# Optimization experiments

Hardware: AMD Instinct MI355X
Metric: run time of the kernel (lower is better)

## Reference

```python
import jax, jax.numpy as jnp
import numpy as np

NL, NH, H, FF, V, P = 12, 12, 768, 3072, 30522, 512
B, L, S = 4, 512, 8
DH = H // NH


def _layer_norm(x, g, b, eps=1e-12):
    m = x.mean(-1, keepdims=True)
    v = jnp.mean((x - m) ** 2, axis=-1, keepdims=True)
    return (x - m) * jax.lax.rsqrt(v + eps) * g + b


def setup_inputs() -> dict:
    key = jax.random.key(0)
    ks = iter(jax.random.split(key, 40))
    pm = lambda shape: jax.random.normal(next(ks), shape, jnp.float32) * 0.02
    inp = {
        'word_emb': pm((V, H)), 'pos_emb': pm((P, H)), 'type_emb': pm((2, H)),
        'emb_ln_g': jnp.ones((H,), jnp.float32), 'emb_ln_b': jnp.zeros((H,), jnp.float32),
        'Wq': pm((NL, H, H)), 'bq': jnp.zeros((NL, H), jnp.float32),
        'Wk': pm((NL, H, H)), 'bk': jnp.zeros((NL, H), jnp.float32),
        'Wv': pm((NL, H, H)), 'bv': jnp.zeros((NL, H), jnp.float32),
        'Wo': pm((NL, H, H)), 'bo': jnp.zeros((NL, H), jnp.float32),
        'attn_ln_g': jnp.ones((NL, H), jnp.float32), 'attn_ln_b': jnp.zeros((NL, H), jnp.float32),
        'W1': pm((NL, H, FF)), 'b1': jnp.zeros((NL, FF), jnp.float32),
        'W2': pm((NL, FF, H)), 'b2': jnp.zeros((NL, H), jnp.float32),
        'ffn_ln_g': jnp.ones((NL, H), jnp.float32), 'ffn_ln_b': jnp.zeros((NL, H), jnp.float32),
        'fc_w': pm((H,)), 'fc_b': jnp.zeros((), jnp.float32),
    }
    inp['input_ids'] = jax.random.randint(next(ks), (B, L), 0, V)
    inp['token_type_ids'] = jnp.zeros((B, L), jnp.int32)
    # valid-length prefix attention_mask and sorted bos_locations (history = 64)
    vl = np.array([384 + 16 * (i % 8) for i in range(B)])
    hist = 64
    am = (np.arange(L)[None, :] < vl[:, None]).astype(np.int32)
    bos = np.stack([hist + (np.arange(S) * (v - hist)) // S for v in vl]).astype(np.int64)
    inp['attention_mask'] = jnp.asarray(am)
    inp['bos_locations'] = jnp.asarray(bos)
    return inp


def _forward(word_emb, pos_emb, type_emb, emb_ln_g, emb_ln_b,
             Wq, bq, Wk, bk, Wv, bv, Wo, bo, attn_ln_g, attn_ln_b,
             W1, b1, W2, b2, ffn_ln_g, ffn_ln_b, fc_w, fc_b,
             input_ids, token_type_ids, attention_mask, bos_locations):
    Bs, Ls = input_ids.shape
    t = jnp.arange(Ls)
    valid_len = attention_mask.sum(-1)                       # [B]
    hist = bos_locations[:, 0]                               # [B] history length
    # segment id per token: number of bos positions <= t, minus 1 (-1 in history)
    seg = (bos_locations[:, :, None] <= t[None, None, :]).sum(1) - 1   # [B,L]
    valid = t[None, :] < valid_len[:, None]                  # [B,L]
    # block-diagonal candidate attention mask (history rows/cols fully visible)
    p = t[None, :, None]
    q = t[None, None, :]
    hist_pq = (p < hist[:, None, None]) | (q < hist[:, None, None])
    same_seg = seg[:, :, None] == seg[:, None, :]
    mask = valid[:, :, None] & valid[:, None, :] & (hist_pq | same_seg)  # [B,L,L]
    bias = jnp.where(mask, 0.0, -10000.0).astype(jnp.float32)[:, None, :, :]  # [B,1,L,L]

    # BERT embeddings
    x = word_emb[input_ids] + pos_emb[t][None] + type_emb[token_type_ids]
    x = _layer_norm(x, emb_ln_g, emb_ln_b)
    scale = 1.0 / jnp.sqrt(jnp.asarray(DH, x.dtype))

    for l in range(NL):
        qh = (x @ Wq[l] + bq[l]).reshape(Bs, Ls, NH, DH)
        kh = (x @ Wk[l] + bk[l]).reshape(Bs, Ls, NH, DH)
        vh = (x @ Wv[l] + bv[l]).reshape(Bs, Ls, NH, DH)
        scores = jnp.einsum('bqhd,bkhd->bhqk', qh, kh) * scale + bias
        probs = jax.nn.softmax(scores, axis=-1)
        ctx = jnp.einsum('bhqk,bkhd->bqhd', probs, vh).reshape(Bs, Ls, H)
        x = _layer_norm(x + ctx @ Wo[l] + bo[l], attn_ln_g[l], attn_ln_b[l])
        h = jax.nn.gelu(x @ W1[l] + b1[l], approximate=False)
        x = _layer_norm(x + h @ W2[l] + b2[l], ffn_ln_g[l], ffn_ln_b[l])

    # variable-length segment mean pooling via membership matmul
    starts = bos_locations                                   # [B,S]
    ends = jnp.concatenate([bos_locations[:, 1:], valid_len[:, None]], axis=1)
    memb = ((t[None, None, :] >= starts[:, :, None]) &
            (t[None, None, :] < ends[:, :, None])).astype(x.dtype)        # [B,S,L]
    pooled = jnp.einsum('bsl,bld->bsd', memb, x) / memb.sum(-1, keepdims=True)
    logits = pooled @ fc_w + fc_b                            # [B,S]
    return jnp.squeeze(logits)


def reference(word_emb, pos_emb, type_emb, emb_ln_g, emb_ln_b,
              Wq, bq, Wk, bk, Wv, bv, Wo, bo, attn_ln_g, attn_ln_b,
              W1, b1, W2, b2, ffn_ln_g, ffn_ln_b, fc_w, fc_b,
              input_ids, token_type_ids, attention_mask, bos_locations):
    return _forward(word_emb, pos_emb, type_emb, emb_ln_g, emb_ln_b,
                    Wq, bq, Wk, bk, Wv, bv, Wo, bo, attn_ln_g, attn_ln_b,
                    W1, b1, W2, b2, ffn_ln_g, ffn_ln_b, fc_w, fc_b,
                    input_ids, token_type_ids, attention_mask, bos_locations)
```

## Files before the change

### kernel.cpp

```cpp
#include <hip/hip_runtime.h>
#include <math.h>

#define HH 768
#define FF 3072
#define NL 12
#define NH 12
#define DH 64
#define BB 4
#define LL 512
#define SS 8
#define MM (BB*LL)
#define WQSZ (HH*HH)
#define W1SZ (HH*FF)
#define LWB 7077888
#define OFF_WO 1769472
#define OFF_W1 2359296
#define OFF_W2 4718592

typedef short bf16x8 __attribute__((ext_vector_type(8)));
typedef float f32x4 __attribute__((ext_vector_type(4)));

__device__ inline ushort f2b(float f) {
  unsigned u = __float_as_uint(f);
  unsigned r = (u + 0x7FFFu + ((u >> 16) & 1u)) >> 16;
  return (ushort)r;
}

__device__ inline void swz_xy(int& x, int& y) {
  int gx = gridDim.x, gy = gridDim.y;
  int flat = blockIdx.x + blockIdx.y * gx;
  int nwg = gx * gy;
  int q = nwg >> 3, r = nwg & 7;
  int xcd = flat & 7, off = flat >> 3;
  int wgid = (xcd < r ? xcd * (q + 1) : r * (q + 1) + (xcd - r) * q) + off;
  x = wgid / gy; y = wgid - x * gy;
}

__global__ void prep_kernel(const int* __restrict__ am, const int* __restrict__ bos,
                            int* __restrict__ seg, int* __restrict__ vl) {
  int b = blockIdx.x;
  int t = threadIdx.x;
  __shared__ int red[512];
  red[t] = am[b*LL + t];
  __syncthreads();
  for (int off = 256; off > 0; off >>= 1) {
    if (t < off) red[t] += red[t+off];
    __syncthreads();
  }
  if (t == 0) vl[b] = red[0];
  int cnt = 0;
  #pragma unroll
  for (int s = 0; s < SS; s++) cnt += (bos[b*SS + s] <= t) ? 1 : 0;
  seg[b*LL + t] = cnt - 1;
}

__global__ __launch_bounds__(256) void embed_ln_kernel(
    const float* __restrict__ word_emb, const float* __restrict__ pos_emb,
    const float* __restrict__ type_emb, const float* __restrict__ g,
    const float* __restrict__ bta, const int* __restrict__ ids,
    const int* __restrict__ tts, float* __restrict__ x, ushort* __restrict__ xb)
{
  int row = blockIdx.x;
  int l = row & (LL-1);
  int t = threadIdx.x;
  int id = ids[row];
  int ty = tts[row];
  float v[3];
  float s = 0.f, sq = 0.f;
  #pragma unroll
  for (int j = 0; j < 3; j++) {
    int c = t + j*256;
    float val = word_emb[(size_t)id*HH + c] + pos_emb[l*HH + c] + type_emb[ty*HH + c];
    v[j] = val; s += val; sq += val*val;
  }
  __shared__ float rs[256], rq[256];
  rs[t] = s; rq[t] = sq;
  __syncthreads();
  for (int off = 128; off > 0; off >>= 1) {
    if (t < off) { rs[t] += rs[t+off]; rq[t] += rq[t+off]; }
    __syncthreads();
  }
  float mean = rs[0] / HH;
  float var  = rq[0] / HH - mean*mean;
  float inv  = rsqrtf(var + 1e-12f);
  #pragma unroll
  for (int j = 0; j < 3; j++) {
    int c = t + j*256;
    float o = (v[j]-mean)*inv*g[c] + bta[c];
    x[(size_t)row*HH + c] = o;
    xb[(size_t)row*HH + c] = f2b(o);
  }
}

template<int NP>
__global__ __launch_bounds__(256) void add_ln_kernel(
    const float* __restrict__ xin, const float* __restrict__ y,
    const float* __restrict__ g, const float* __restrict__ bta,
    float* __restrict__ xout, ushort* __restrict__ xb)
{
  int row = blockIdx.x;
  int t = threadIdx.x;
  float v[3];
  float s = 0.f, sq = 0.f;
  #pragma unroll
  for (int j = 0; j < 3; j++) {
    int c = t + j*256;
    size_t ix = (size_t)row*HH + c;
    float val = xin[ix];
    #pragma unroll
    for (int p = 0; p < NP; p++) val += y[(size_t)p*MM*HH + ix];
    v[j] = val; s += val; sq += val*val;
  }
  __shared__ float rs[256], rq[256];
  rs[t] = s; rq[t] = sq;
  __syncthreads();
  for (int off = 128; off > 0; off >>= 1) {
    if (t < off) { rs[t] += rs[t+off]; rq[t] += rq[t+off]; }
    __syncthreads();
  }
  float mean = rs[0] / HH;
  float var  = rq[0] / HH - mean*mean;
  float inv  = rsqrtf(var + 1e-12f);
  #pragma unroll
  for (int j = 0; j < 3; j++) {
    int c = t + j*256;
    float o = (v[j]-mean)*inv*g[c] + bta[c];
    xout[(size_t)row*HH + c] = o;
    xb[(size_t)row*HH + c] = f2b(o);
  }
}

__global__ __launch_bounds__(256) void convw_all_kernel(
    const float* __restrict__ Wq, const float* __restrict__ Wk,
    const float* __restrict__ Wv, const float* __restrict__ Wo,
    const float* __restrict__ W1, const float* __restrict__ W2,
    ushort* __restrict__ wbuf)
{
  int idx = blockIdx.x;
  int l = idx / 1728;
  int t0 = idx % 1728;
  size_t base = (size_t)l * LWB;
  const float* src; ushort* dst; int Nsrc, dstK, k0, n0src, n0dst;
  if (t0 < 432) {
    int nt = t0 / 12, kt = t0 % 12;
    int z = nt / 12, ntl = nt % 12;
    src = (z == 0 ? Wq : z == 1 ? Wk : Wv) + (size_t)l*WQSZ;
    dst = wbuf + base;
    Nsrc = HH; dstK = HH; k0 = kt*64; n0src = ntl*64; n0dst = nt*64;
  } else if (t0 < 576) {
    int t = t0 - 432; int nt = t / 12, kt = t % 12;
    src = Wo + (size_t)l*WQSZ;
    dst = wbuf + base + OFF_WO;
    Nsrc = HH; dstK = HH; k0 = kt*64; n0src = n0dst = nt*64;
  } else if (t0 < 1152) {
    int t = t0 - 576; int nt = t / 12, kt = t % 12;
    src = W1 + (size_t)l*W1SZ;
    dst = wbuf + base + OFF_W1;
    Nsrc = FF; dstK = HH; k0 = kt*64; n0src = n0dst = nt*64;
  } else {
    int t = t0 - 1152; int nt = t / 48, kt = t % 48;
    src = W2 + (size_t)l*W1SZ;
    dst = wbuf + base + OFF_W2;
    Nsrc = HH; dstK = FF; k0 = kt*64; n0src = n0dst = nt*64;
  }
  __shared__ ushort tt[64][72];
  int tid = threadIdx.x;
  int r = tid >> 4, c = (tid & 15) << 2;
  #pragma unroll
  for (int i = 0; i < 4; i++) {
    int rr = r + i*16;
    float4 v = *(const float4*)&src[(size_t)(k0+rr)*Nsrc + n0src + c];
    tt[c+0][rr] = f2b(v.x); tt[c+1][rr] = f2b(v.y);
    tt[c+2][rr] = f2b(v.z); tt[c+3][rr] = f2b(v.w);
  }
  __syncthreads();
  #pragma unroll
  for (int it = 0; it < 2; it++) {
    int n = it*32 + (tid >> 3);
    int k = (tid & 7) << 3;
    ushort tmp8[8];
    #pragma unroll
    for (int j = 0; j < 8; j++) tmp8[j] = tt[n][k+j];
    *(uint4*)&dst[(size_t)(n0dst+n)*dstK + k0 + k] = *(const uint4*)tmp8;
  }
}

template<int MODE>
__global__ __launch_bounds__(256) void gemm_bt(
    const ushort* __restrict__ A, const ushort* __restrict__ Bt,
    const float* __restrict__ ba, const float* __restrict__ bb,
    const float* __restrict__ bc, float* __restrict__ Cf,
    ushort* __restrict__ Cb, int M, int N, int K)
{
  __shared__ __align__(16) ushort As[2][128*64];
  __shared__ __align__(16) ushort Bs[2][64*64];
  const int tid = threadIdx.x;
  const int lane = tid & 63, wid = tid >> 6;
  const int wm = wid >> 1, wn = wid & 1;
  int bx, by; swz_xy(bx, by);
  const int m0 = by * 128, n0 = bx * 64;
  int kbeg = 0, kcnt = K;
  if (MODE == 2) { kcnt = K >> 2; kbeg = blockIdx.z * kcnt; }
  const int NT = kcnt >> 6;

  auto STAGE = [&](int buf, int k0) {
    #pragma unroll
    for (int j = 0; j < 4; j++) {
      int c = j*256 + tid;
      int r = c >> 3;
      int kk = ((c & 7) ^ (r & 7)) << 3;
      __builtin_amdgcn_global_load_lds(
        (const __attribute__((address_space(1))) void*)(A + (size_t)(m0+r)*K + k0 + kk),
        (__attribute__((address_space(3))) void*)(&As[buf][c*8]), 16, 0, 0);
    }
    #pragma unroll
    for (int j = 0; j < 2; j++) {
      int c = j*256 + tid;
      int r = c >> 3;
      int kk = ((c & 7) ^ (r & 7)) << 3;
      __builtin_amdgcn_global_load_lds(
        (const __attribute__((address_space(1))) void*)(Bt + (size_t)(n0+r)*K + k0 + kk),
        (__attribute__((address_space(3))) void*)(&Bs[buf][c*8]), 16, 0, 0);
    }
  };

  f32x4 acc[4][2] = {};
  STAGE(0, kbeg);
  __syncthreads();
  int cur = 0;
  for (int t = 0; t < NT; ++t) {
    if (t + 1 < NT) STAGE(cur ^ 1, kbeg + (t+1)*64);
    bf16x8 af[4][2], bfv[2][2];
    #pragma unroll
    for (int mi = 0; mi < 4; mi++) {
      int row = wm*64 + mi*16 + (lane & 15);
      #pragma unroll
      for (int ks = 0; ks < 2; ks++) {
        int kb = (ks*64 + ((lane >> 4) << 4)) ^ ((row & 7) << 4);
        af[mi][ks] = *(const bf16x8*)((const char*)&As[cur][0] + row*128 + kb);
      }
    }
    #pragma unroll
    for (int ni = 0; ni < 2; ni++) {
      int row = wn*32 + ni*16 + (lane & 15);
      #pragma unroll
      for (int ks = 0; ks < 2; ks++) {
        int kb = (ks*64 + ((lane >> 4) << 4)) ^ ((row & 7) << 4);
        bfv[ni][ks] = *(const bf16x8*)((const char*)&Bs[cur][0] + row*128 + kb);
      }
    }
    #pragma unroll
    for (int ks = 0; ks < 2; ks++)
      #pragma unroll
      for (int mi = 0; mi < 4; mi++)
        #pragma unroll
        for (int ni = 0; ni < 2; ni++)
          acc[mi][ni] = __builtin_amdgcn_mfma_f32_16x16x32_bf16(af[mi][ks], bfv[ni][ks], acc[mi][ni], 0, 0, 0);
    __syncthreads();
    cur ^= 1;
  }

  #pragma unroll
  for (int mi = 0; mi < 4; mi++) {
    #pragma unroll
    for (int ni = 0; ni < 2; ni++) {
      int col = n0 + wn*32 + ni*16 + (lane & 15);
      if (MODE == 0) {
        int z = n0 / 768;
        int cc = col - z*768;
        float bvv = (z == 0 ? ba : z == 1 ? bb : bc)[cc];
        #pragma unroll
        for (int r = 0; r < 4; r++) {
          int row = m0 + wm*64 + mi*16 + (lane >> 4)*4 + r;
          Cb[(size_t)z*MM*HH + (size_t)row*HH + cc] = f2b(acc[mi][ni][r] + bvv);
        }
      } else if (MODE == 1) {
        float bvv = ba[col];
        #pragma unroll
        for (int r = 0; r < 4; r++) {
          int row = m0 + wm*64 + mi*16 + (lane >> 4)*4 + r;
          float v = acc[mi][ni][r] + bvv;
          v = 0.5f * v * (1.0f + erff(v * 0.70710678118654752f));
          Cb[(size_t)row*N + col] = f2b(v);
        }
      } else {
        float bvv = (blockIdx.z == 0) ? ba[col] : 0.f;
        #pragma unroll
        for (int r = 0; r < 4; r++) {
          int row = m0 + wm*64 + mi*16 + (lane >> 4)*4 + r;
          Cf[(size_t)blockIdx.z*M*N + (size_t)row*N + col] = acc[mi][ni][r] + bvv;
        }
      }
    }
  }
}

__global__ __launch_bounds__(256) void attn_mfma_kernel(
    const ushort* __restrict__ Q, const ushort* __restrict__ Kp, const ushort* __restrict__ Vp,
    ushort* __restrict__ ctx, const int* __restrict__ seg, const int* __restrict__ vl,
    const int* __restrict__ bos)
{
  const int q0 = blockIdx.x * 64;
  const int h  = blockIdx.y;
  const int b  = blockIdx.z;
  const int tid = threadIdx.x;
  const int lane = tid & 63;
  const int wid = tid >> 6;

  __shared__ __align__(16) char Ks[8192];
  __shared__ __align__(16) char Vt[8192];
  __shared__ __align__(16) char Ps[4][2048];
  __shared__ int segk[64];

  const int qrow_frag = q0 + wid*16 + (lane & 15);
  bf16x8 qf[2];
  #pragma unroll
  for (int c = 0; c < 2; c++)
    qf[c] = *(const bf16x8*)&Q[((size_t)(b*LL + qrow_frag))*HH + h*DH + 32*c + (lane >> 4)*8];

  const int vlb  = vl[b];
  const int hist = bos[b*SS];
  int segq[4]; bool qvalid[4], qhist[4];
  #pragma unroll
  for (int r = 0; r < 4; r++) {
    int qg = q0 + wid*16 + (lane >> 4)*4 + r;
    segq[r]   = seg[b*LL + qg];
    qvalid[r] = qg < vlb;
    qhist[r]  = qg < hist;
  }

  float mrow[4], lrow[4];
  #pragma unroll
  for (int r = 0; r < 4; r++) { mrow[r] = -1e30f; lrow[r] = 0.f; }
  f32x4 Oacc[4] = {};

  for (int k0 = 0; k0 < LL; k0 += 64) {
    __syncthreads();
    #pragma unroll
    for (int p = 0; p < 2; p++) {
      int r  = (tid >> 3) + 32*p;
      int c8 = (tid & 7) * 8;
      uint4 kv = *(const uint4*)&Kp[((size_t)(b*LL + k0 + r))*HH + h*DH + c8];
      *(uint4*)(Ks + (r*128 + ((c8*2) ^ ((r & 7) << 4)))) = kv;
    }
    #pragma unroll
    for (int p = 0; p < 2; p++) {
      int k  = lane;
      int d0 = wid*8 + 32*p;
      uint4 vv = *(const uint4*)&Vp[((size_t)(b*LL + k0 + k))*HH + h*DH + d0];
      const ushort* pv = (const ushort*)&vv;
      #pragma unroll
      for (int j = 0; j < 8; j++) {
        int d = d0 + j;
        *(ushort*)(Vt + (d*128 + ((k*2) ^ ((d & 7) << 4)))) = pv[j];
      }
    }
    if (tid < 64) segk[tid] = seg[b*LL + k0 + tid];
    __syncthreads();

    f32x4 sacc[4] = {};
    #pragma unroll
    for (int t = 0; t < 4; t++) {
      int krow = (lane & 15) + 16*t;
      #pragma unroll
      for (int c = 0; c < 2; c++) {
        bf16x8 kf = *(const bf16x8*)(Ks + (krow*128 +
                      (((32*c + (lane >> 4)*8)*2) ^ ((krow & 7) << 4))));
        sacc[t] = __builtin_amdgcn_mfma_f32_16x16x32_bf16(qf[c], kf, sacc[t], 0, 0, 0);
      }
    }

    #pragma unroll
    for (int t = 0; t < 4; t++) {
      int kg = k0 + (lane & 15) + 16*t;
      bool kvalid = kg < vlb;
      bool khist  = kg < hist;
      int  sk     = segk[(lane & 15) + 16*t];
      #pragma unroll
      for (int r = 0; r < 4; r++) {
        bool ok = qvalid[r] && kvalid && (khist || qhist[r] || (segq[r] == sk));
        sacc[t][r] = sacc[t][r]*0.125f + (ok ? 0.f : -10000.f);
      }
    }

    float scl[4];
    #pragma unroll
    for (int r = 0; r < 4; r++) {
      float rm = fmaxf(fmaxf(sacc[0][r], sacc[1][r]), fmaxf(sacc[2][r], sacc[3][r]));
      rm = fmaxf(rm, __shfl_xor(rm, 1));
      rm = fmaxf(rm, __shfl_xor(rm, 2));
      rm = fmaxf(rm, __shfl_xor(rm, 4));
      rm = fmaxf(rm, __shfl_xor(rm, 8));
      float mnew = fmaxf(mrow[r], rm);
      scl[r] = __expf(mrow[r] - mnew);
      float rsum = 0.f;
      #pragma unroll
      for (int t = 0; t < 4; t++) {
        float p = __expf(sacc[t][r] - mnew);
        sacc[t][r] = p;
        rsum += p;
      }
      rsum += __shfl_xor(rsum, 1);
      rsum += __shfl_xor(rsum, 2);
      rsum += __shfl_xor(rsum, 4);
      rsum += __shfl_xor(rsum, 8);
      mrow[r] = mnew;
      lrow[r] = lrow[r]*scl[r] + rsum;
    }

    char* Pl = Ps[wid];
    #pragma unroll
    for (int t = 0; t < 4; t++) {
      #pragma unroll
      for (int r = 0; r < 4; r++) {
        int q = (lane >> 4)*4 + r;
        int k = (lane & 15) + 16*t;
        *(ushort*)(Pl + (q*128 + ((k*2) ^ ((q & 7) << 4)))) = f2b(sacc[t][r]);
      }
    }
    asm volatile("s_waitcnt lgkmcnt(0)" ::: "memory");
    bf16x8 pf[2];
    #pragma unroll
    for (int c = 0; c < 2; c++) {
      int q = lane & 15;
      int k = 32*c + (lane >> 4)*8;
      pf[c] = *(const bf16x8*)(Pl + (q*128 + ((k*2) ^ ((q & 7) << 4))));
    }

    #pragma unroll
    for (int nt = 0; nt < 4; nt++) {
      #pragma unroll
      for (int r = 0; r < 4; r++) Oacc[nt][r] *= scl[r];
      int d = (lane & 15) + 16*nt;
      #pragma unroll
      for (int c = 0; c < 2; c++) {
        int k = 32*c + (lane >> 4)*8;
        bf16x8 vf = *(const bf16x8*)(Vt + (d*128 + ((k*2) ^ ((d & 7) << 4))));
        Oacc[nt] = __builtin_amdgcn_mfma_f32_16x16x32_bf16(pf[c], vf, Oacc[nt], 0, 0, 0);
      }
    }
  }

  #pragma unroll
  for (int nt = 0; nt < 4; nt++) {
    #pragma unroll
    for (int r = 0; r < 4; r++) {
      int q = q0 + wid*16 + (lane >> 4)*4 + r;
      int d = h*DH + (lane & 15) + 16*nt;
      ctx[(size_t)(b*LL + q)*HH + d] = f2b(Oacc[nt][r] / lrow[r]);
    }
  }
}

__global__ __launch_bounds__(256) void rowdot_kernel(const float* __restrict__ x,
                                                     const float* __restrict__ w,
                                                     float* __restrict__ rd) {
  int row = blockIdx.x;
  int t = threadIdx.x;
  float s = 0.f;
  #pragma unroll
  for (int j = 0; j < 3; j++) {
    int c = t + j*256;
    s = fmaf(x[(size_t)row*HH + c], w[c], s);
  }
  __shared__ float red[256];
  red[t] = s;
  __syncthreads();
  for (int off = 128; off > 0; off >>= 1) {
    if (t < off) red[t] += red[t+off];
    __syncthreads();
  }
  if (t == 0) rd[row] = red[0];
}

__global__ void logits_kernel(const float* __restrict__ rd, const int* __restrict__ bos,
                              const int* __restrict__ vl, const float* __restrict__ fcb,
                              float* __restrict__ out) {
  int i = threadIdx.x;
  if (i >= BB*SS) return;
  int b = i / SS, s = i % SS;
  int start = bos[b*SS + s];
  int end   = (s == SS-1) ? vl[b] : bos[b*SS + s + 1];
  float sum = 0.f;
  for (int t = start; t < end; t++) sum += rd[b*LL + t];
  out[i] = sum / (float)(end - start) + fcb[0];
}

extern "C" void kernel_launch(void* const* d_in, const int* in_sizes, int n_in,
                              void* d_out, int out_size, void* d_ws, size_t ws_size,
                              hipStream_t stream) {
  const float* word_emb  = (const float*)d_in[0];
  const float* pos_emb   = (const float*)d_in[1];
  const float* type_emb  = (const float*)d_in[2];
  const float* emb_ln_g  = (const float*)d_in[3];
  const float* emb_ln_b  = (const float*)d_in[4];
  const float* Wq        = (const float*)d_in[5];
  const float* bq        = (const float*)d_in[6];
  const float* Wk        = (const float*)d_in[7];
  const float* bk        = (const float*)d_in[8];
  const float* Wv        = (const float*)d_in[9];
  const float* bv        = (const float*)d_in[10];
  const float* Wo        = (const float*)d_in[11];
  const float* bo        = (const float*)d_in[12];
  const float* attn_ln_g = (const float*)d_in[13];
  const float* attn_ln_b = (const float*)d_in[14];
  const float* W1        = (const float*)d_in[15];
  const float* b1        = (const float*)d_in[16];
  const float* W2        = (const float*)d_in[17];
  const float* b2        = (const float*)d_in[18];
  const float* ffn_ln_g  = (const float*)d_in[19];
  const float* ffn_ln_b  = (const float*)d_in[20];
  const float* fc_w      = (const float*)d_in[21];
  const float* fc_b      = (const float*)d_in[22];
  const int* input_ids   = (const int*)d_in[23];
  const int* token_type  = (const int*)d_in[24];
  const int* am          = (const int*)d_in[25];
  const int* bos         = (const int*)d_in[26];
  float* out = (float*)d_out;

  char* w = (char*)d_ws;
  float*  x       = (float*)w;  w += (size_t)MM*HH*4;
  float*  tmp     = (float*)w;  w += (size_t)4*MM*HH*4;
  ushort* qkv_bf  = (ushort*)w; w += (size_t)3*MM*HH*2;
  ushort* x_bf    = (ushort*)w; w += (size_t)MM*HH*2;
  ushort* ctx_bf  = (ushort*)w; w += (size_t)MM*HH*2;
  ushort* hbuf_bf = (ushort*)w; w += (size_t)MM*FF*2;
  ushort* wbuf    = (ushort*)w; w += (size_t)NL*LWB*2;
  float*  rd      = (float*)w;  w += (size_t)MM*4;
  int*    seg     = (int*)w;    w += (size_t)MM*4;
  int*    vl      = (int*)w;    w += 64;

  prep_kernel<<<BB, 512, 0, stream>>>(am, bos, seg, vl);
  convw_all_kernel<<<NL*1728, 256, 0, stream>>>(Wq, Wk, Wv, Wo, W1, W2, wbuf);
  embed_ln_kernel<<<MM, 256, 0, stream>>>(word_emb, pos_emb, type_emb,
                                          emb_ln_g, emb_ln_b, input_ids, token_type, x, x_bf);

  dim3 gqkv(2304/64, MM/128);
  dim3 g_ff1(FF/64, MM/128);
  dim3 g_sk(HH/64, MM/128, 4);
  dim3 gattn(LL/64, NH, BB);

  for (int l = 0; l < NL; l++) {
    const ushort* Wqkv_t = wbuf + (size_t)l*LWB;
    const ushort* Wo_t   = wbuf + (size_t)l*LWB + OFF_WO;
    const ushort* W1_t   = wbuf + (size_t)l*LWB + OFF_W1;
    const ushort* W2_t   = wbuf + (size_t)l*LWB + OFF_W2;

    gemm_bt<0><<<gqkv, 256, 0, stream>>>(x_bf, Wqkv_t,
        bq + (size_t)l*HH, bk + (size_t)l*HH, bv + (size_t)l*HH,
        nullptr, qkv_bf, MM, 2304, HH);

    attn_mfma_kernel<<<gattn, 256, 0, stream>>>(qkv_bf, qkv_bf + (size_t)MM*HH,
                                                qkv_bf + (size_t)2*MM*HH, ctx_bf, seg, vl, bos);

    gemm_bt<2><<<g_sk, 256, 0, stream>>>(ctx_bf, Wo_t,
        bo + (size_t)l*HH, nullptr, nullptr, tmp, nullptr, MM, HH, HH);

    add_ln_kernel<4><<<MM, 256, 0, stream>>>(x, tmp, attn_ln_g + (size_t)l*HH,
                                             attn_ln_b + (size_t)l*HH, x, x_bf);

    gemm_bt<1><<<g_ff1, 256, 0, stream>>>(x_bf, W1_t,
        b1 + (size_t)l*FF, nullptr, nullptr, nullptr, hbuf_bf, MM, FF, HH);

    gemm_bt<2><<<g_sk, 256, 0, stream>>>(hbuf_bf, W2_t,
        b2 + (size_t)l*HH, nullptr, nullptr, tmp, nullptr, MM, HH, FF);

    add_ln_kernel<4><<<MM, 256, 0, stream>>>(x, tmp, ffn_ln_g + (size_t)l*HH,
                                             ffn_ln_b + (size_t)l*HH, x, x_bf);
  }

  rowdot_kernel<<<MM, 256, 0, stream>>>(x, fc_w, rd);
  logits_kernel<<<1, 64, 0, stream>>>(rd, bos, vl, fc_b, out);
}
```

Measured before the change: 1.460 ms.

## Double-buffer K/V tiles in attention and rework weight transpose smem layout

The attention kernel now prefetches the next K/V tile and segment ids into registers while computing on the current tile, then stores them into a second shared-memory buffer, so there is one barrier per iteration instead of two. The goal is to hide global-load latency behind the MFMA work. The weight-conversion kernel also changes its transpose staging: it writes packed ushort2 values along rows and reads columns, using a different padding. In exchange the attention kernel uses more LDS and registers, which may lower occupancy.

```diff
diff --git a/kernel.cpp b/kernel.cpp
--- a/kernel.cpp
+++ b/kernel.cpp
@@ -163,25 +163,28 @@
     dst = wbuf + base + OFF_W2;
     Nsrc = HH; dstK = FF; k0 = kt*64; n0src = n0dst = nt*64;
   }
-  __shared__ ushort tt[64][72];
+  __shared__ ushort tt[64][66];
   int tid = threadIdx.x;
-  int r = tid >> 4, c = (tid & 15) << 2;
+  int kr = tid >> 4;
+  int n0 = (tid & 15) << 2;
   #pragma unroll
   for (int i = 0; i < 4; i++) {
-    int rr = r + i*16;
-    float4 v = *(const float4*)&src[(size_t)(k0+rr)*Nsrc + n0src + c];
-    tt[c+0][rr] = f2b(v.x); tt[c+1][rr] = f2b(v.y);
-    tt[c+2][rr] = f2b(v.z); tt[c+3][rr] = f2b(v.w);
+    int k = kr + i*16;
+    float4 v = *(const float4*)&src[(size_t)(k0+k)*Nsrc + n0src + n0];
+    ushort2 lo = { f2b(v.x), f2b(v.y) };
+    ushort2 hi = { f2b(v.z), f2b(v.w) };
+    *(ushort2*)&tt[k][n0]     = lo;
+    *(ushort2*)&tt[k][n0 + 2] = hi;
   }
   __syncthreads();
   #pragma unroll
   for (int it = 0; it < 2; it++) {
-    int n = it*32 + (tid >> 3);
-    int k = (tid & 7) << 3;
+    int n  = it*32 + (tid >> 3);
+    int kc = (tid & 7) << 3;
     ushort tmp8[8];
     #pragma unroll
-    for (int j = 0; j < 8; j++) tmp8[j] = tt[n][k+j];
-    *(uint4*)&dst[(size_t)(n0dst+n)*dstK + k0 + k] = *(const uint4*)tmp8;
+    for (int j = 0; j < 8; j++) tmp8[j] = tt[kc + j][n];
+    *(uint4*)&dst[(size_t)(n0dst + n)*dstK + k0 + kc] = *(const uint4*)tmp8;
   }
 }
 
@@ -307,10 +310,10 @@
   const int lane = tid & 63;
   const int wid = tid >> 6;
 
-  __shared__ __align__(16) char Ks[8192];
-  __shared__ __align__(16) char Vt[8192];
+  __shared__ __align__(16) char Ks[2][8192];
+  __shared__ __align__(16) char Vt[2][8192];
   __shared__ __align__(16) char Ps[4][2048];
-  __shared__ int segk[64];
+  __shared__ int segk[2][64];
 
   const int qrow_frag = q0 + wid*16 + (lane & 15);
   bf16x8 qf[2];
@@ -334,29 +337,45 @@
   for (int r = 0; r < 4; r++) { mrow[r] = -1e30f; lrow[r] = 0.f; }
   f32x4 Oacc[4] = {};
 
-  for (int k0 = 0; k0 < LL; k0 += 64) {
-    __syncthreads();
-    #pragma unroll
-    for (int p = 0; p < 2; p++) {
-      int r  = (tid >> 3) + 32*p;
-      int c8 = (tid & 7) * 8;
-      uint4 kv = *(const uint4*)&Kp[((size_t)(b*LL + k0 + r))*HH + h*DH + c8];
-      *(uint4*)(Ks + (r*128 + ((c8*2) ^ ((r & 7) << 4)))) = kv;
-    }
-    #pragma unroll
-    for (int p = 0; p < 2; p++) {
-      int k  = lane;
-      int d0 = wid*8 + 32*p;
-      uint4 vv = *(const uint4*)&Vp[((size_t)(b*LL + k0 + k))*HH + h*DH + d0];
-      const ushort* pv = (const ushort*)&vv;
-      #pragma unroll
-      for (int j = 0; j < 8; j++) {
-        int d = d0 + j;
-        *(ushort*)(Vt + (d*128 + ((k*2) ^ ((d & 7) << 4)))) = pv[j];
-      }
-    }
-    if (tid < 64) segk[tid] = seg[b*LL + k0 + tid];
-    __syncthreads();
+  uint4 kreg0, kreg1, vreg0, vreg1;
+  int sreg = 0;
+
+  auto LOADT = [&](int k0) {
+    int rk = tid >> 3;
+    int c8 = (tid & 7) * 8;
+    kreg0 = *(const uint4*)&Kp[((size_t)(b*LL + k0 + rk))*HH + h*DH + c8];
+    kreg1 = *(const uint4*)&Kp[((size_t)(b*LL + k0 + rk + 32))*HH + h*DH + c8];
+    vreg0 = *(const uint4*)&Vp[((size_t)(b*LL + k0 + lane))*HH + h*DH + wid*8];
+    vreg1 = *(const uint4*)&Vp[((size_t)(b*LL + k0 + lane))*HH + h*DH + wid*8 + 32];
+    if (tid < 64) sreg = seg[b*LL + k0 + tid];
+  };
+  auto STORET = [&](int buf) {
+    int rk = tid >> 3;
+    int c8 = (tid & 7) * 8;
+    *(uint4*)(Ks[buf] + (rk*128 + ((c8*2) ^ ((rk & 7) << 4)))) = kreg0;
+    int rk2 = rk + 32;
+    *(uint4*)(Ks[buf] + (rk2*128 + ((c8*2) ^ ((rk2 & 7) << 4)))) = kreg1;
+    const ushort* pv0 = (const ushort*)&vreg0;
+    const ushort* pv1 = (const ushort*)&vreg1;
+    #pragma unroll
+    for (int j = 0; j < 8; j++) {
+      int d  = wid*8 + j;
+      *(ushort*)(Vt[buf] + (d*128 + ((lane*2) ^ ((d & 7) << 4)))) = pv0[j];
+      int d2 = d + 32;
+      *(ushort*)(Vt[buf] + (d2*128 + ((lane*2) ^ ((d2 & 7) << 4)))) = pv1[j];
+    }
+    if (tid < 64) segk[buf][tid] = sreg;
+  };
+
+  LOADT(0);
+  STORET(0);
+  __syncthreads();
+
+  for (int kt = 0; kt < 8; kt++) {
+    const int cur = kt & 1;
+    const int k0 = kt * 64;
+    if (kt < 7) LOADT(k0 + 64);
+    __builtin_amdgcn_sched_barrier(0);
 
     f32x4 sacc[4] = {};
     #pragma unroll
@@ -364,7 +383,7 @@
       int krow = (lane & 15) + 16*t;
       #pragma unroll
       for (int c = 0; c < 2; c++) {
-        bf16x8 kf = *(const bf16x8*)(Ks + (krow*128 +
+        bf16x8 kf = *(const bf16x8*)(Ks[cur] + (krow*128 +
                       (((32*c + (lane >> 4)*8)*2) ^ ((krow & 7) << 4))));
         sacc[t] = __builtin_amdgcn_mfma_f32_16x16x32_bf16(qf[c], kf, sacc[t], 0, 0, 0);
       }
@@ -375,7 +394,7 @@
       int kg = k0 + (lane & 15) + 16*t;
       bool kvalid = kg < vlb;
       bool khist  = kg < hist;
-      int  sk     = segk[(lane & 15) + 16*t];
+      int  sk     = segk[cur][(lane & 15) + 16*t];
       #pragma unroll
       for (int r = 0; r < 4; r++) {
         bool ok = qvalid[r] && kvalid && (khist || qhist[r] || (segq[r] == sk));
@@ -435,10 +454,13 @@
       #pragma unroll
       for (int c = 0; c < 2; c++) {
         int k = 32*c + (lane >> 4)*8;
-        bf16x8 vf = *(const bf16x8*)(Vt + (d*128 + ((k*2) ^ ((d & 7) << 4))));
+        bf16x8 vf = *(const bf16x8*)(Vt[cur] + (d*128 + ((k*2) ^ ((d & 7) << 4))));
         Oacc[nt] = __builtin_amdgcn_mfma_f32_16x16x32_bf16(pf[c], vf, Oacc[nt], 0, 0, 0);
       }
     }
+
+    if (kt < 7) STORET(cur ^ 1);
+    __syncthreads();
   }
 
   #pragma unroll
```

After: 1.428 ms. -2.1%, faster.
